# Optimization experiments

Hardware: AMD Instinct MI355X
Metric: run time of the kernel (lower is better)

Reference implementation:

```python
import jax, jax.numpy as jnp
from jax import lax
import numpy as np

B, T, D_IN, H, D_L1_IN = 128, 2048, 5, 128, 256


def _gru_layer(x, w_ih, w_hh, b_ih, b_hh, reverse):
    # x: [B,T,D]; w_ih: [3H,D]; w_hh: [3H,H]. PyTorch gate order: r, z, n.
    gx = jnp.einsum('btd,gd->btg', x, w_ih) + b_ih  # [B,T,3H] input projections, batched
    if reverse:
        gx = gx[:, ::-1]
    gx_t = jnp.swapaxes(gx, 0, 1)  # [T,B,3H]
    h0 = jnp.zeros((x.shape[0], H), x.dtype)

    def step(h, gxt):
        gh = h @ w_hh.T + b_hh  # [B,3H]
        r = jax.nn.sigmoid(gxt[:, :H] + gh[:, :H])
        z = jax.nn.sigmoid(gxt[:, H:2 * H] + gh[:, H:2 * H])
        n = jnp.tanh(gxt[:, 2 * H:] + r * gh[:, 2 * H:])
        h_new = (1.0 - z) * n + z * h
        return h_new, h_new

    _, ys = lax.scan(step, h0, gx_t)  # ys: [T,B,H]
    ys = jnp.swapaxes(ys, 0, 1)  # [B,T,H]
    if reverse:
        ys = ys[:, ::-1]
    return ys


def setup_inputs() -> dict:
    key = jax.random.key(0)
    ks = jax.random.split(key, 16)
    s0 = 1.0 / np.sqrt(H)

    def w(k, shape):
        return jax.random.uniform(k, shape, jnp.float32, -s0, s0)

    inp = {'seq': jax.random.normal(ks[0], (B, T, D_IN), jnp.float32)}
    # layer 0 forward / backward (input dim 5)
    inp['w_ih_l0f'] = w(ks[1], (3 * H, D_IN)); inp['w_hh_l0f'] = w(ks[2], (3 * H, H))
    inp['b_ih_l0f'] = w(ks[3], (3 * H,));      inp['b_hh_l0f'] = w(ks[4], (3 * H,))
    inp['w_ih_l0b'] = w(ks[5], (3 * H, D_IN)); inp['w_hh_l0b'] = w(ks[6], (3 * H, H))
    inp['b_ih_l0b'] = w(ks[7], (3 * H,));      inp['b_hh_l0b'] = w(ks[8], (3 * H,))
    # layer 1 forward / backward (input dim 256 = 2*H)
    inp['w_ih_l1f'] = w(ks[9], (3 * H, D_L1_IN));  inp['w_hh_l1f'] = w(ks[10], (3 * H, H))
    inp['b_ih_l1f'] = w(ks[11], (3 * H,));         inp['b_hh_l1f'] = w(ks[12], (3 * H,))
    inp['w_ih_l1b'] = w(ks[13], (3 * H, D_L1_IN)); inp['w_hh_l1b'] = w(ks[14], (3 * H, H))
    inp['b_ih_l1b'] = w(ks[15], (3 * H,));         inp['b_hh_l1b'] = w(ks[15], (3 * H,)) * 0.9
    # linear head
    kf = jax.random.split(ks[0], 2)
    inp['fc_w'] = w(kf[0], (1, 2 * H))
    inp['fc_b'] = w(kf[1], (1,))
    return inp


def reference(seq, w_ih_l0f, w_hh_l0f, b_ih_l0f, b_hh_l0f,
              w_ih_l0b, w_hh_l0b, b_ih_l0b, b_hh_l0b,
              w_ih_l1f, w_hh_l1f, b_ih_l1f, b_hh_l1f,
              w_ih_l1b, w_hh_l1b, b_ih_l1b, b_hh_l1b,
              fc_w, fc_b):
    # layer 0: bidirectional, concat directions
    y0f = _gru_layer(seq, w_ih_l0f, w_hh_l0f, b_ih_l0f, b_hh_l0f, reverse=False)
    y0b = _gru_layer(seq, w_ih_l0b, w_hh_l0b, b_ih_l0b, b_hh_l0b, reverse=True)
    y0 = jnp.concatenate([y0f, y0b], axis=-1)  # [B,T,256]
    # layer 1
    y1f = _gru_layer(y0, w_ih_l1f, w_hh_l1f, b_ih_l1f, b_hh_l1f, reverse=False)
    y1b = _gru_layer(y0, w_ih_l1b, w_hh_l1b, b_ih_l1b, b_hh_l1b, reverse=True)
    y1 = jnp.concatenate([y1f, y1b], axis=-1)  # [B,T,256]
    # head on last timestep
    return y1[:, -1, :] @ fc_w.T + fc_b  # [B,1]
```

## Files before the change

### kernel.cpp

```cpp
#include <hip/hip_runtime.h>
#include <hip/hip_fp16.h>
#include <cstdint>

#define B_   128
#define T_   2048
#define DIN  5
#define H_   128
#define G3   384
#define D1   256
#define CH   256
#define NCH  (T_ / CH)

typedef _Float16 half8 __attribute__((ext_vector_type(8)));
typedef float f32x4 __attribute__((ext_vector_type(4)));

__device__ __forceinline__ float sigmoid_f(float x) {
    return __builtin_amdgcn_rcpf(1.0f + __expf(-x));
}
__device__ __forceinline__ float tanh_f(float x) {
    return 1.0f - 2.0f * __builtin_amdgcn_rcpf(__expf(2.0f * x) + 1.0f);
}
__device__ __forceinline__ unsigned long long pack4h(const float* h) {
    union { __half2 h2[2]; unsigned long long u; } pk;
    pk.h2[0] = __floats2half2_rn(h[0], h[1]);
    pk.h2[1] = __floats2half2_rn(h[2], h[3]);
    return pk.u;
}
__device__ __forceinline__ f32x4 h4_to_f(unsigned long long u) {
    union { unsigned long long u; __half2 h2[2]; } p; p.u = u;
    const float2 a = __half22float2(p.h2[0]);
    const float2 b = __half22float2(p.h2[1]);
    f32x4 r; r[0] = a.x; r[1] = a.y; r[2] = b.x; r[3] = b.y; return r;
}
__device__ __forceinline__ void fast_barrier() {
    asm volatile("s_waitcnt lgkmcnt(0)\n\ts_barrier" ::: "memory");
}

__global__ __launch_bounds__(256, 1) void scan0_mfma3(
    const float* __restrict__ seq,
    const float* __restrict__ wihf, const float* __restrict__ whhf,
    const float* __restrict__ bihf, const float* __restrict__ bhhf,
    const float* __restrict__ wihb, const float* __restrict__ whhb,
    const float* __restrict__ bihb, const float* __restrict__ bhhb,
    __half* __restrict__ y0)
{
    const int tid = threadIdx.x;
    const int w  = tid >> 6;
    const int l  = tid & 63;
    const int lo = l & 15;
    const int g  = l >> 4;
    const int dir = blockIdx.x >> 3;
    const int bg  = blockIdx.x & 7;

    const float* w_ih = dir ? wihb : wihf;
    const float* w_hh = dir ? whhb : whhf;
    const float* b_ih = dir ? bihb : bihf;
    const float* b_hh = dir ? bhhb : bhhf;

    __shared__ __align__(16) char smem[2 * 16 * 512];

    half8 a_r[2][5], a_z[2][5], a_n[2][5], a_x[2];
#pragma unroll
    for (int i = 0; i < 2; ++i) {
        const int grow = (2 * w + i) * 16 + lo;
#pragma unroll
        for (int c = 0; c < 5; ++c) {
            half8 vr, vz, vn;
#pragma unroll
            for (int j = 0; j < 8; ++j) {
                const int k = c * 32 + g * 8 + j;
                float fr, fz, fn;
                if (k < 128) {
                    fr = w_hh[grow * H_ + k];
                    fz = w_hh[(128 + grow) * H_ + k];
                    fn = w_hh[(256 + grow) * H_ + k];
                } else if (k < 133) {
                    fr = w_ih[grow * DIN + (k - 128)];
                    fz = w_ih[(128 + grow) * DIN + (k - 128)];
                    fn = 0.f;
                } else if (k == 133) {
                    fr = b_ih[grow] + b_hh[grow];
                    fz = b_ih[128 + grow] + b_hh[128 + grow];
                    fn = b_hh[256 + grow];
                } else { fr = 0.f; fz = 0.f; fn = 0.f; }
                vr[j] = (_Float16)fr; vz[j] = (_Float16)fz; vn[j] = (_Float16)fn;
            }
            a_r[i][c] = vr; a_z[i][c] = vz; a_n[i][c] = vn;
        }
        half8 vx;
#pragma unroll
        for (int j = 0; j < 8; ++j) {
            const int k = 128 + g * 8 + j;
            float f = 0.f;
            if (k < 133)       f = w_ih[(256 + grow) * DIN + (k - 128)];
            else if (k == 133) f = b_ih[256 + grow];
            vx[j] = (_Float16)f;
        }
        a_x[i] = vx;
    }

#pragma unroll
    for (int q = 0; q < 4; ++q) {
        f32x4 z = {0.f, 0.f, 0.f, 0.f};
        *reinterpret_cast<f32x4*>(smem + tid * 64 + q * 16) = z;
    }
    __syncthreads();
    if (tid < 32) {
        const int row = tid & 15, bu = tid >> 4;
        *(_Float16*)(smem + bu * 8192 + row * 512 + (266 ^ ((row & 7) << 4))) =
            (_Float16)1.0f;
    }
    const bool stager = tid < 80;
    const int sb = tid / 5, sd = tid % 5;
    const size_t seqbase = (size_t)(bg * 16 + sb) * T_ * DIN + sd;
    float x_t1 = 0.f;
    if (stager) {
        const int tt0 = dir ? (T_ - 1) : 0;
        const float x0 = seq[seqbase + (size_t)tt0 * DIN];
        *(_Float16*)(smem + sb * 512 + ((256 + 2 * sd) ^ ((sb & 7) << 4))) =
            (_Float16)x0;
        const int tt1 = dir ? (T_ - 2) : 1;
        x_t1 = seq[seqbase + (size_t)tt1 * DIN];
    }
    __syncthreads();

    float h_old[2][4];
#pragma unroll
    for (int i = 0; i < 2; ++i)
#pragma unroll
        for (int q = 0; q < 4; ++q) h_old[i][q] = 0.f;

    for (int t = 0; t < T_; ++t) {
        char* cur = smem + (t & 1) * 8192;
        char* nxt = smem + ((t + 1) & 1) * 8192;

        if (stager)
            *(_Float16*)(nxt + sb * 512 + ((256 + 2 * sd) ^ ((sb & 7) << 4))) =
                (_Float16)x_t1;

        half8 bf[5];
#pragma unroll
        for (int c = 0; c < 5; ++c)
            bf[c] = *reinterpret_cast<const half8*>(
                cur + lo * 512 + ((c * 64 + g * 16) ^ ((lo & 7) << 4)));

        float x_t2 = 0.f;
        if (stager) {
            const int t2 = (t + 2 < T_) ? t + 2 : T_ - 1;
            const int tt2 = dir ? (T_ - 1 - t2) : t2;
            x_t2 = seq[seqbase + (size_t)tt2 * DIN];
        }

        f32x4 accr[2], accz[2], accn[2], accx[2];
#pragma unroll
        for (int i = 0; i < 2; ++i) {
            f32x4 zr = {0.f, 0.f, 0.f, 0.f};
            accr[i] = zr; accz[i] = zr; accn[i] = zr;
#pragma unroll
            for (int c = 0; c < 5; ++c) {
                accr[i] = __builtin_amdgcn_mfma_f32_16x16x32_f16(a_r[i][c], bf[c], accr[i], 0, 0, 0);
                accz[i] = __builtin_amdgcn_mfma_f32_16x16x32_f16(a_z[i][c], bf[c], accz[i], 0, 0, 0);
                accn[i] = __builtin_amdgcn_mfma_f32_16x16x32_f16(a_n[i][c], bf[c], accn[i], 0, 0, 0);
            }
            accx[i] = __builtin_amdgcn_mfma_f32_16x16x32_f16(a_x[i], bf[4], zr, 0, 0, 0);
        }

        const int tt = dir ? (T_ - 1 - t) : t;
#pragma unroll
        for (int i = 0; i < 2; ++i) {
            float hn[4];
#pragma unroll
            for (int q = 0; q < 4; ++q) {
                const float r = sigmoid_f(accr[i][q]);
                const float z = sigmoid_f(accz[i][q]);
                const float n = tanh_f(accx[i][q] + r * accn[i][q]);
                hn[q] = n + z * (h_old[i][q] - n);
                h_old[i][q] = hn[q];
            }
            const int j0 = (2 * w + i) * 16 + g * 4;
            const unsigned long long pu = pack4h(hn);
            *reinterpret_cast<unsigned long long*>(
                &y0[((size_t)(bg * 16 + lo) * T_ + tt) * D1 + dir * H_ + j0]) = pu;
            *reinterpret_cast<unsigned long long*>(
                nxt + lo * 512 + ((2 * j0) ^ ((lo & 7) << 4))) = pu;
        }
        x_t1 = x_t2;
        fast_barrier();
    }
}

__global__ __launch_bounds__(256, 2) void gemm1_f16(
    const __half* __restrict__ A,
    const float* __restrict__ W,
    const float* __restrict__ bias,
    __half* __restrict__ C,
    int c0)
{
    __shared__ __align__(16) _Float16 As[128][32];
    __shared__ __align__(16) _Float16 Bs[64][32];
    const int tid = threadIdx.x;
    const int wave = tid >> 6, l = tid & 63;
    const int wm = wave >> 1, wn = wave & 1;
    const int lo = l & 15, g = l >> 4;
    const int m0 = blockIdx.x * 128, n0 = blockIdx.y * 64;

    f32x4 acc[4][2];
#pragma unroll
    for (int mt = 0; mt < 4; ++mt)
#pragma unroll
        for (int nt = 0; nt < 2; ++nt) {
            f32x4 z = {0.f, 0.f, 0.f, 0.f};
            acc[mt][nt] = z;
        }

    for (int kc = 0; kc < 256; kc += 32) {
#pragma unroll
        for (int r2 = 0; r2 < 2; ++r2) {
            const int idx = tid + r2 * 256;
            const int row = idx >> 2, seg = idx & 3;
            const int m = m0 + row, bb = m >> 8, tlq = m & (CH - 1);
            const __half* src = A + ((size_t)bb * T_ + c0 + tlq) * D1 + kc + seg * 8;
            *reinterpret_cast<uint4*>(&As[row][seg * 8]) =
                *reinterpret_cast<const uint4*>(src);
        }
        {
            const int row = tid >> 2, seg = tid & 3;
            const float* srcw = W + (size_t)(n0 + row) * D1 + kc + seg * 8;
            const float4 u0 = *reinterpret_cast<const float4*>(srcw);
            const float4 u1 = *reinterpret_cast<const float4*>(srcw + 4);
            half8 hv;
            hv[0] = (_Float16)u0.x; hv[1] = (_Float16)u0.y;
            hv[2] = (_Float16)u0.z; hv[3] = (_Float16)u0.w;
            hv[4] = (_Float16)u1.x; hv[5] = (_Float16)u1.y;
            hv[6] = (_Float16)u1.z; hv[7] = (_Float16)u1.w;
            *reinterpret_cast<half8*>(&Bs[row][seg * 8]) = hv;
        }
        __syncthreads();
        half8 af[4], bfr[2];
#pragma unroll
        for (int mt = 0; mt < 4; ++mt)
            af[mt] = *reinterpret_cast<half8*>(&As[wm * 64 + mt * 16 + lo][g * 8]);
#pragma unroll
        for (int nt = 0; nt < 2; ++nt)
            bfr[nt] = *reinterpret_cast<half8*>(&Bs[wn * 32 + nt * 16 + lo][g * 8]);
#pragma unroll
        for (int mt = 0; mt < 4; ++mt)
#pragma unroll
            for (int nt = 0; nt < 2; ++nt)
                acc[mt][nt] = __builtin_amdgcn_mfma_f32_16x16x32_f16(
                    af[mt], bfr[nt], acc[mt][nt], 0, 0, 0);
        __syncthreads();
    }
#pragma unroll
    for (int nt = 0; nt < 2; ++nt) {
        const int n = n0 + wn * 32 + nt * 16 + lo;
        const float bv = bias[n];
#pragma unroll
        for (int mt = 0; mt < 4; ++mt) {
            const int mrow = m0 + wm * 64 + mt * 16 + g * 4;
#pragma unroll
            for (int q = 0; q < 4; ++q)
                C[(size_t)(mrow + q) * G3 + n] = __float2half(acc[mt][nt][q] + bv);
        }
    }
}

__global__ __launch_bounds__(256, 1) void scan1_mfma3(
    const __half* __restrict__ gxc,
    const float* __restrict__ whh, const float* __restrict__ bhh,
    float* __restrict__ h1, int c)
{
    const int tid = threadIdx.x;
    const int w = tid >> 6, l = tid & 63;
    const int lo = l & 15, g = l >> 4;
    const int grp = blockIdx.x;

    __shared__ __align__(16) char smem[2 * 16 * 256];

    half8 a_r[2][4], a_z[2][4], a_n[2][4];
    float br[2][4], bz[2][4], bn[2][4];
#pragma unroll
    for (int i = 0; i < 2; ++i) {
        const int grow = (2 * w + i) * 16 + lo;
#pragma unroll
        for (int cc = 0; cc < 4; ++cc) {
            half8 vr, vz, vn;
#pragma unroll
            for (int j = 0; j < 8; ++j) {
                const int k = cc * 32 + g * 8 + j;
                vr[j] = (_Float16)whh[grow * H_ + k];
                vz[j] = (_Float16)whh[(128 + grow) * H_ + k];
                vn[j] = (_Float16)whh[(256 + grow) * H_ + k];
            }
            a_r[i][cc] = vr; a_z[i][cc] = vz; a_n[i][cc] = vn;
        }
#pragma unroll
        for (int q = 0; q < 4; ++q) {
            const int gq = (2 * w + i) * 16 + g * 4 + q;
            br[i][q] = bhh[gq];
            bz[i][q] = bhh[128 + gq];
            bn[i][q] = bhh[256 + gq];
        }
    }

#pragma unroll
    for (int q = 0; q < 2; ++q) {
        f32x4 z = {0.f, 0.f, 0.f, 0.f};
        *reinterpret_cast<f32x4*>(smem + tid * 32 + q * 16) = z;
    }
    __syncthreads();

    float h_old[2][4];
    if (c == 0) {
#pragma unroll
        for (int i = 0; i < 2; ++i)
#pragma unroll
            for (int q = 0; q < 4; ++q) h_old[i][q] = 0.f;
    } else {
#pragma unroll
        for (int i = 0; i < 2; ++i) {
            const int j0 = (2 * w + i) * 16 + g * 4;
            const f32x4 hv = *reinterpret_cast<const f32x4*>(
                &h1[(grp * 16 + lo) * H_ + j0]);
            float hn[4];
#pragma unroll
            for (int q = 0; q < 4; ++q) { h_old[i][q] = hv[q]; hn[q] = hv[q]; }
            *reinterpret_cast<unsigned long long*>(
                smem + lo * 256 + ((2 * j0) ^ ((lo & 7) << 4))) = pack4h(hn);
        }
    }
    __syncthreads();

    const __half* gxl = gxc + (size_t)(grp * 16 + lo) * CH * G3;
    unsigned long long gxc_cur[6], gxc_nxt[6];
#pragma unroll
    for (int i = 0; i < 2; ++i) {
        const int gr0 = (2 * w + i) * 16 + g * 4;
        gxc_cur[i]     = *reinterpret_cast<const unsigned long long*>(gxl + gr0);
        gxc_cur[2 + i] = *reinterpret_cast<const unsigned long long*>(gxl + 128 + gr0);
        gxc_cur[4 + i] = *reinterpret_cast<const unsigned long long*>(gxl + 256 + gr0);
    }

    for (int t = 0; t < CH; ++t) {
        char* curb = smem + (t & 1) * 4096;
        char* nxtb = smem + ((t + 1) & 1) * 4096;

        half8 bf[4];
#pragma unroll
        for (int cc = 0; cc < 4; ++cc)
            bf[cc] = *reinterpret_cast<const half8*>(
                curb + lo * 256 + ((cc * 64 + g * 16) ^ ((lo & 7) << 4)));

        const int tn = (t + 1 < CH) ? t + 1 : t;
        const __half* p = gxl + (size_t)tn * G3;
#pragma unroll
        for (int i = 0; i < 2; ++i) {
            const int gr0 = (2 * w + i) * 16 + g * 4;
            gxc_nxt[i]     = *reinterpret_cast<const unsigned long long*>(p + gr0);
            gxc_nxt[2 + i] = *reinterpret_cast<const unsigned long long*>(p + 128 + gr0);
            gxc_nxt[4 + i] = *reinterpret_cast<const unsigned long long*>(p + 256 + gr0);
        }

        f32x4 accr[2], accz[2], accn[2];
#pragma unroll
        for (int i = 0; i < 2; ++i) {
            f32x4 zr = {0.f, 0.f, 0.f, 0.f};
            accr[i] = zr; accz[i] = zr; accn[i] = zr;
#pragma unroll
            for (int cc = 0; cc < 4; ++cc) {
                accr[i] = __builtin_amdgcn_mfma_f32_16x16x32_f16(a_r[i][cc], bf[cc], accr[i], 0, 0, 0);
                accz[i] = __builtin_amdgcn_mfma_f32_16x16x32_f16(a_z[i][cc], bf[cc], accz[i], 0, 0, 0);
                accn[i] = __builtin_amdgcn_mfma_f32_16x16x32_f16(a_n[i][cc], bf[cc], accn[i], 0, 0, 0);
            }
        }

#pragma unroll
        for (int i = 0; i < 2; ++i) {
            const f32x4 gr = h4_to_f(gxc_cur[i]);
            const f32x4 gz = h4_to_f(gxc_cur[2 + i]);
            const f32x4 gn = h4_to_f(gxc_cur[4 + i]);
            float hn[4];
#pragma unroll
            for (int q = 0; q < 4; ++q) {
                const float r = sigmoid_f(accr[i][q] + br[i][q] + gr[q]);
                const float z = sigmoid_f(accz[i][q] + bz[i][q] + gz[q]);
                const float n = tanh_f(gn[q] + r * (accn[i][q] + bn[i][q]));
                hn[q] = n + z * (h_old[i][q] - n);
                h_old[i][q] = hn[q];
            }
            const int j0 = (2 * w + i) * 16 + g * 4;
            *reinterpret_cast<unsigned long long*>(
                nxtb + lo * 256 + ((2 * j0) ^ ((lo & 7) << 4))) = pack4h(hn);
        }
#pragma unroll
        for (int i = 0; i < 6; ++i) gxc_cur[i] = gxc_nxt[i];
        fast_barrier();
    }

#pragma unroll
    for (int i = 0; i < 2; ++i) {
        const int j0 = (2 * w + i) * 16 + g * 4;
        f32x4 hv;
#pragma unroll
        for (int q = 0; q < 4; ++q) hv[q] = h_old[i][q];
        *reinterpret_cast<f32x4*>(&h1[(grp * 16 + lo) * H_ + j0]) = hv;
    }
}

__global__ __launch_bounds__(384, 1) void back1_fc(
    const __half* __restrict__ y0, const float* __restrict__ h1,
    const float* __restrict__ w_ih_1b, const float* __restrict__ b_ih_1b,
    const float* __restrict__ b_hh_1b,
    const float* __restrict__ fc_w, const float* __restrict__ fc_b,
    float* __restrict__ out)
{
    const int g = threadIdx.x;
    const int b = blockIdx.x;
    __shared__ float ylast[D1];
    __shared__ float pre_rz[2 * H_];
    __shared__ float gxn[H_], ghn[H_];
    __shared__ float hb[H_];
    __shared__ float red[H_];

    if (g < D1) ylast[g] = __half2float(y0[((size_t)b * T_ + (T_ - 1)) * D1 + g]);
    __syncthreads();

    float accb = b_ih_1b[g];
    const float* wrow = w_ih_1b + (size_t)g * D1;
#pragma unroll 8
    for (int k = 0; k < D1; k += 4) {
        const float4 v = *reinterpret_cast<const float4*>(&ylast[k]);
        const float4 wv = *reinterpret_cast<const float4*>(&wrow[k]);
        accb += v.x * wv.x + v.y * wv.y + v.z * wv.z + v.w * wv.w;
    }
    const float bh2 = b_hh_1b[g];
    if (g < 2 * H_) pre_rz[g] = accb + bh2;
    else            { gxn[g - 2 * H_] = accb; ghn[g - 2 * H_] = bh2; }
    __syncthreads();
    if (g < H_) {
        const float r = sigmoid_f(pre_rz[g]);
        const float z = sigmoid_f(pre_rz[g + H_]);
        const float n = tanh_f(gxn[g] + r * ghn[g]);
        hb[g] = (1.0f - z) * n;
    }
    __syncthreads();
    if (g < H_) red[g] = h1[b * H_ + g] * fc_w[g] + hb[g] * fc_w[H_ + g];
    __syncthreads();
    if (g == 0) {
        float s = fc_b[0];
#pragma unroll 8
        for (int k = 0; k < H_; ++k) s += red[k];
        out[b] = s;
    }
}

extern "C" void kernel_launch(void* const* d_in, const int* in_sizes, int n_in,
                              void* d_out, int out_size, void* d_ws, size_t ws_size,
                              hipStream_t stream)
{
    const float* seq      = (const float*)d_in[0];
    const float* w_ih_l0f = (const float*)d_in[1];
    const float* w_hh_l0f = (const float*)d_in[2];
    const float* b_ih_l0f = (const float*)d_in[3];
    const float* b_hh_l0f = (const float*)d_in[4];
    const float* w_ih_l0b = (const float*)d_in[5];
    const float* w_hh_l0b = (const float*)d_in[6];
    const float* b_ih_l0b = (const float*)d_in[7];
    const float* b_hh_l0b = (const float*)d_in[8];
    const float* w_ih_l1f = (const float*)d_in[9];
    const float* w_hh_l1f = (const float*)d_in[10];
    const float* b_ih_l1f = (const float*)d_in[11];
    const float* b_hh_l1f = (const float*)d_in[12];
    const float* w_ih_l1b = (const float*)d_in[13];
    const float* b_ih_l1b = (const float*)d_in[15];
    const float* b_hh_l1b = (const float*)d_in[16];
    const float* fc_w     = (const float*)d_in[17];
    const float* fc_b     = (const float*)d_in[18];
    float* out = (float*)d_out;

    __half* y0h = (__half*)d_ws;
    __half* gxc = (__half*)((char*)d_ws +
                  (size_t)B_ * T_ * D1 * sizeof(__half));
    float*  h1  = (float*)(gxc + (size_t)B_ * CH * G3);

    hipLaunchKernelGGL(scan0_mfma3, dim3(16), dim3(256), 0, stream,
        seq, w_ih_l0f, w_hh_l0f, b_ih_l0f, b_hh_l0f,
             w_ih_l0b, w_hh_l0b, b_ih_l0b, b_hh_l0b, y0h);

    for (int ci = 0; ci < NCH; ++ci) {
        hipLaunchKernelGGL(gemm1_f16, dim3(B_ * CH / 128, 6), dim3(256), 0, stream,
            y0h, w_ih_l1f, b_ih_l1f, gxc, ci * CH);
        hipLaunchKernelGGL(scan1_mfma3, dim3(8), dim3(256), 0, stream,
            gxc, w_hh_l1f, b_hh_l1f, h1, ci);
    }

    hipLaunchKernelGGL(back1_fc, dim3(B_), dim3(384), 0, stream,
        y0h, h1, w_ih_l1b, b_ih_l1b, b_hh_l1b, fc_w, fc_b, out);
}
```

Before: 3.666 ms.

## Split recurrent scans across eight waves with one gate tile per wave

Both recurrent scan kernels now launch 512 threads (8 waves), and each wave owns a single 16-row gate tile rather than two. The aim is to shorten the serial per-timestep chain of MFMAs and gate math each wave runs, spreading it across more SIMDs. The cost is a barrier across more waves on every timestep, and the 8 extra waves read the same shared h buffer. The scan0 stager logic and the zeroing of shared memory are adjusted to match the new thread count.

After: 3.890 ms. +6.1%, slower.

```diff
diff --git a/kernel.cpp b/kernel.cpp
--- a/kernel.cpp
+++ b/kernel.cpp
@@ -36,7 +36,7 @@
     asm volatile("s_waitcnt lgkmcnt(0)\n\ts_barrier" ::: "memory");
 }
 
-__global__ __launch_bounds__(256, 1) void scan0_mfma3(
+__global__ __launch_bounds__(512, 2) void scan0_mfma4(
     const float* __restrict__ seq,
     const float* __restrict__ wihf, const float* __restrict__ whhf,
     const float* __restrict__ bihf, const float* __restrict__ bhhf,
@@ -59,10 +59,9 @@
 
     __shared__ __align__(16) char smem[2 * 16 * 512];
 
-    half8 a_r[2][5], a_z[2][5], a_n[2][5], a_x[2];
-#pragma unroll
-    for (int i = 0; i < 2; ++i) {
-        const int grow = (2 * w + i) * 16 + lo;
+    half8 a_r[5], a_z[5], a_n[5], a_x;
+    {
+        const int grow = w * 16 + lo;
 #pragma unroll
         for (int c = 0; c < 5; ++c) {
             half8 vr, vz, vn;
@@ -85,7 +84,7 @@
                 } else { fr = 0.f; fz = 0.f; fn = 0.f; }
                 vr[j] = (_Float16)fr; vz[j] = (_Float16)fz; vn[j] = (_Float16)fn;
             }
-            a_r[i][c] = vr; a_z[i][c] = vz; a_n[i][c] = vn;
+            a_r[c] = vr; a_z[c] = vz; a_n[c] = vn;
         }
         half8 vx;
 #pragma unroll
@@ -96,13 +95,13 @@
             else if (k == 133) f = b_ih[256 + grow];
             vx[j] = (_Float16)f;
         }
-        a_x[i] = vx;
-    }
-
-#pragma unroll
-    for (int q = 0; q < 4; ++q) {
+        a_x = vx;
+    }
+
+#pragma unroll
+    for (int q = 0; q < 2; ++q) {
         f32x4 z = {0.f, 0.f, 0.f, 0.f};
-        *reinterpret_cast<f32x4*>(smem + tid * 64 + q * 16) = z;
+        *reinterpret_cast<f32x4*>(smem + tid * 32 + q * 16) = z;
     }
     __syncthreads();
     if (tid < 32) {
@@ -124,11 +123,9 @@
     }
     __syncthreads();
 
-    float h_old[2][4];
-#pragma unroll
-    for (int i = 0; i < 2; ++i)
-#pragma unroll
-        for (int q = 0; q < 4; ++q) h_old[i][q] = 0.f;
+    float h_old[4];
+#pragma unroll
+    for (int q = 0; q < 4; ++q) h_old[q] = 0.f;
 
     for (int t = 0; t < T_; ++t) {
         char* cur = smem + (t & 1) * 8192;
@@ -151,33 +148,28 @@
             x_t2 = seq[seqbase + (size_t)tt2 * DIN];
         }
 
-        f32x4 accr[2], accz[2], accn[2], accx[2];
-#pragma unroll
-        for (int i = 0; i < 2; ++i) {
-            f32x4 zr = {0.f, 0.f, 0.f, 0.f};
-            accr[i] = zr; accz[i] = zr; accn[i] = zr;
-#pragma unroll
-            for (int c = 0; c < 5; ++c) {
-                accr[i] = __builtin_amdgcn_mfma_f32_16x16x32_f16(a_r[i][c], bf[c], accr[i], 0, 0, 0);
-                accz[i] = __builtin_amdgcn_mfma_f32_16x16x32_f16(a_z[i][c], bf[c], accz[i], 0, 0, 0);
-                accn[i] = __builtin_amdgcn_mfma_f32_16x16x32_f16(a_n[i][c], bf[c], accn[i], 0, 0, 0);
+        f32x4 zr = {0.f, 0.f, 0.f, 0.f};
+        f32x4 accr = zr, accz = zr, accn = zr, accx;
+#pragma unroll
+        for (int c = 0; c < 5; ++c) {
+            accr = __builtin_amdgcn_mfma_f32_16x16x32_f16(a_r[c], bf[c], accr, 0, 0, 0);
+            accz = __builtin_amdgcn_mfma_f32_16x16x32_f16(a_z[c], bf[c], accz, 0, 0, 0);
+            accn = __builtin_amdgcn_mfma_f32_16x16x32_f16(a_n[c], bf[c], accn, 0, 0, 0);
+        }
+        accx = __builtin_amdgcn_mfma_f32_16x16x32_f16(a_x, bf[4], zr, 0, 0, 0);
+
+        const int tt = dir ? (T_ - 1 - t) : t;
+        {
+            float hn[4];
+#pragma unroll
+            for (int q = 0; q < 4; ++q) {
+                const float r = sigmoid_f(accr[q]);
+                const float z = sigmoid_f(accz[q]);
+                const float n = tanh_f(accx[q] + r * accn[q]);
+                hn[q] = n + z * (h_old[q] - n);
+                h_old[q] = hn[q];
             }
-            accx[i] = __builtin_amdgcn_mfma_f32_16x16x32_f16(a_x[i], bf[4], zr, 0, 0, 0);
-        }
-
-        const int tt = dir ? (T_ - 1 - t) : t;
-#pragma unroll
-        for (int i = 0; i < 2; ++i) {
-            float hn[4];
-#pragma unroll
-            for (int q = 0; q < 4; ++q) {
-                const float r = sigmoid_f(accr[i][q]);
-                const float z = sigmoid_f(accz[i][q]);
-                const float n = tanh_f(accx[i][q] + r * accn[i][q]);
-                hn[q] = n + z * (h_old[i][q] - n);
-                h_old[i][q] = hn[q];
-            }
-            const int j0 = (2 * w + i) * 16 + g * 4;
+            const int j0 = w * 16 + g * 4;
             const unsigned long long pu = pack4h(hn);
             *reinterpret_cast<unsigned long long*>(
                 &y0[((size_t)(bg * 16 + lo) * T_ + tt) * D1 + dir * H_ + j0]) = pu;
@@ -265,7 +257,7 @@
     }
 }
 
-__global__ __launch_bounds__(256, 1) void scan1_mfma3(
+__global__ __launch_bounds__(512, 2) void scan1_mfma4(
     const __half* __restrict__ gxc,
     const float* __restrict__ whh, const float* __restrict__ bhh,
     float* __restrict__ h1, int c)
@@ -277,11 +269,10 @@
 
     __shared__ __align__(16) char smem[2 * 16 * 256];
 
-    half8 a_r[2][4], a_z[2][4], a_n[2][4];
-    float br[2][4], bz[2][4], bn[2][4];
-#pragma unroll
-    for (int i = 0; i < 2; ++i) {
-        const int grow = (2 * w + i) * 16 + lo;
+    half8 a_r[4], a_z[4], a_n[4];
+    float br[4], bz[4], bn[4];
+    {
+        const int grow = w * 16 + lo;
 #pragma unroll
         for (int cc = 0; cc < 4; ++cc) {
             half8 vr, vz, vn;
@@ -292,53 +283,46 @@
                 vz[j] = (_Float16)whh[(128 + grow) * H_ + k];
                 vn[j] = (_Float16)whh[(256 + grow) * H_ + k];
             }
-            a_r[i][cc] = vr; a_z[i][cc] = vz; a_n[i][cc] = vn;
+            a_r[cc] = vr; a_z[cc] = vz; a_n[cc] = vn;
         }
 #pragma unroll
         for (int q = 0; q < 4; ++q) {
-            const int gq = (2 * w + i) * 16 + g * 4 + q;
-            br[i][q] = bhh[gq];
-            bz[i][q] = bhh[128 + gq];
-            bn[i][q] = bhh[256 + gq];
-        }
-    }
-
-#pragma unroll
-    for (int q = 0; q < 2; ++q) {
+            const int gq = w * 16 + g * 4 + q;
+            br[q] = bhh[gq];
+            bz[q] = bhh[128 + gq];
+            bn[q] = bhh[256 + gq];
+        }
+    }
+
+    {
         f32x4 z = {0.f, 0.f, 0.f, 0.f};
-        *reinterpret_cast<f32x4*>(smem + tid * 32 + q * 16) = z;
-    }
-    __syncthreads();
-
-    float h_old[2][4];
+        *reinterpret_cast<f32x4*>(smem + tid * 16) = z;
+    }
+    __syncthreads();
+
+    float h_old[4];
     if (c == 0) {
 #pragma unroll
-        for (int i = 0; i < 2; ++i)
-#pragma unroll
-            for (int q = 0; q < 4; ++q) h_old[i][q] = 0.f;
+        for (int q = 0; q < 4; ++q) h_old[q] = 0.f;
     } else {
-#pragma unroll
-        for (int i = 0; i < 2; ++i) {
-            const int j0 = (2 * w + i) * 16 + g * 4;
-            const f32x4 hv = *reinterpret_cast<const f32x4*>(
-                &h1[(grp * 16 + lo) * H_ + j0]);
-            float hn[4];
-#pragma unroll
-            for (int q = 0; q < 4; ++q) { h_old[i][q] = hv[q]; hn[q] = hv[q]; }
-            *reinterpret_cast<unsigned long long*>(
-                smem + lo * 256 + ((2 * j0) ^ ((lo & 7) << 4))) = pack4h(hn);
-        }
+        const int j0 = w * 16 + g * 4;
+        const f32x4 hv = *reinterpret_cast<const f32x4*>(
+            &h1[(grp * 16 + lo) * H_ + j0]);
+        float hn[4];
+#pragma unroll
+        for (int q = 0; q < 4; ++q) { h_old[q] = hv[q]; hn[q] = hv[q]; }
+        *reinterpret_cast<unsigned long long*>(
+            smem + lo * 256 + ((2 * j0) ^ ((lo & 7) << 4))) = pack4h(hn);
     }
     __syncthreads();
 
     const __half* gxl = gxc + (size_t)(grp * 16 + lo) * CH * G3;
-    unsigned long long gxc_cur[6], gxc_nxt[6];
-#pragma unroll
-    for (int i = 0; i < 2; ++i) {
-        const int gr0 = (2 * w + i) * 16 + g * 4;
-        gxc_cur[i]     = *reinterpret_cast<const unsigned long long*>(gxl + gr0);
-        gxc_cur[2 + i] = *reinterpret_cast<const unsigned long long*>(gxl + 128 + gr0);
-        gxc_cur[4 + i] = *reinterpret_cast<const unsigned long long*>(gxl + 256 + gr0);
+    unsigned long long gxc_cur[3], gxc_nxt[3];
+    {
+        const int gr0 = w * 16 + g * 4;
+        gxc_cur[0] = *reinterpret_cast<const unsigned long long*>(gxl + gr0);
+        gxc_cur[1] = *reinterpret_cast<const unsigned long long*>(gxl + 128 + gr0);
+        gxc_cur[2] = *reinterpret_cast<const unsigned long long*>(gxl + 256 + gr0);
     }
 
     for (int t = 0; t < CH; ++t) {
@@ -353,56 +337,49 @@
 
         const int tn = (t + 1 < CH) ? t + 1 : t;
         const __half* p = gxl + (size_t)tn * G3;
-#pragma unroll
-        for (int i = 0; i < 2; ++i) {
-            const int gr0 = (2 * w + i) * 16 + g * 4;
-            gxc_nxt[i]     = *reinterpret_cast<const unsigned long long*>(p + gr0);
-            gxc_nxt[2 + i] = *reinterpret_cast<const unsigned long long*>(p + 128 + gr0);
-            gxc_nxt[4 + i] = *reinterpret_cast<const unsigned long long*>(p + 256 + gr0);
-        }
-
-        f32x4 accr[2], accz[2], accn[2];
-#pragma unroll
-        for (int i = 0; i < 2; ++i) {
-            f32x4 zr = {0.f, 0.f, 0.f, 0.f};
-            accr[i] = zr; accz[i] = zr; accn[i] = zr;
-#pragma unroll
-            for (int cc = 0; cc < 4; ++cc) {
-                accr[i] = __builtin_amdgcn_mfma_f32_16x16x32_f16(a_r[i][cc], bf[cc], accr[i], 0, 0, 0);
-                accz[i] = __builtin_amdgcn_mfma_f32_16x16x32_f16(a_z[i][cc], bf[cc], accz[i], 0, 0, 0);
-                accn[i] = __builtin_amdgcn_mfma_f32_16x16x32_f16(a_n[i][cc], bf[cc], accn[i], 0, 0, 0);
+        {
+            const int gr0 = w * 16 + g * 4;
+            gxc_nxt[0] = *reinterpret_cast<const unsigned long long*>(p + gr0);
+            gxc_nxt[1] = *reinterpret_cast<const unsigned long long*>(p + 128 + gr0);
+            gxc_nxt[2] = *reinterpret_cast<const unsigned long long*>(p + 256 + gr0);
+        }
+
+        f32x4 zr = {0.f, 0.f, 0.f, 0.f};
+        f32x4 accr = zr, accz = zr, accn = zr;
+#pragma unroll
+        for (int cc = 0; cc < 4; ++cc) {
+            accr = __builtin_amdgcn_mfma_f32_16x16x32_f16(a_r[cc], bf[cc], accr, 0, 0, 0);
+            accz = __builtin_amdgcn_mfma_f32_16x16x32_f16(a_z[cc], bf[cc], accz, 0, 0, 0);
+            accn = __builtin_amdgcn_mfma_f32_16x16x32_f16(a_n[cc], bf[cc], accn, 0, 0, 0);
+        }
+
+        {
+            const f32x4 gr = h4_to_f(gxc_cur[0]);
+            const f32x4 gz = h4_to_f(gxc_cur[1]);
+            const f32x4 gn = h4_to_f(gxc_cur[2]);
+            float hn[4];
+#pragma unroll
+            for (int q = 0; q < 4; ++q) {
+                const float r = sigmoid_f(accr[q] + br[q] + gr[q]);
+                const float z = sigmoid_f(accz[q] + bz[q] + gz[q]);
+                const float n = tanh_f(gn[q] + r * (accn[q] + bn[q]));
+                hn[q] = n + z * (h_old[q] - n);
+                h_old[q] = hn[q];
             }
-        }
-
-#pragma unroll
-        for (int i = 0; i < 2; ++i) {
-            const f32x4 gr = h4_to_f(gxc_cur[i]);
-            const f32x4 gz = h4_to_f(gxc_cur[2 + i]);
-            const f32x4 gn = h4_to_f(gxc_cur[4 + i]);
-            float hn[4];
-#pragma unroll
-            for (int q = 0; q < 4; ++q) {
-                const float r = sigmoid_f(accr[i][q] + br[i][q] + gr[q]);
-                const float z = sigmoid_f(accz[i][q] + bz[i][q] + gz[q]);
-                const float n = tanh_f(gn[q] + r * (accn[i][q] + bn[i][q]));
-                hn[q] = n + z * (h_old[i][q] - n);
-                h_old[i][q] = hn[q];
-            }
-            const int j0 = (2 * w + i) * 16 + g * 4;
+            const int j0 = w * 16 + g * 4;
             *reinterpret_cast<unsigned long long*>(
                 nxtb + lo * 256 + ((2 * j0) ^ ((lo & 7) << 4))) = pack4h(hn);
         }
 #pragma unroll
-        for (int i = 0; i < 6; ++i) gxc_cur[i] = gxc_nxt[i];
+        for (int i = 0; i < 3; ++i) gxc_cur[i] = gxc_nxt[i];
         fast_barrier();
     }
 
-#pragma unroll
-    for (int i = 0; i < 2; ++i) {
-        const int j0 = (2 * w + i) * 16 + g * 4;
+    {
+        const int j0 = w * 16 + g * 4;
         f32x4 hv;
 #pragma unroll
-        for (int q = 0; q < 4; ++q) hv[q] = h_old[i][q];
+        for (int q = 0; q < 4; ++q) hv[q] = h_old[q];
         *reinterpret_cast<f32x4*>(&h1[(grp * 16 + lo) * H_ + j0]) = hv;
     }
 }
@@ -483,14 +460,14 @@
                   (size_t)B_ * T_ * D1 * sizeof(__half));
     float*  h1  = (float*)(gxc + (size_t)B_ * CH * G3);
 
-    hipLaunchKernelGGL(scan0_mfma3, dim3(16), dim3(256), 0, stream,
+    hipLaunchKernelGGL(scan0_mfma4, dim3(16), dim3(512), 0, stream,
         seq, w_ih_l0f, w_hh_l0f, b_ih_l0f, b_hh_l0f,
              w_ih_l0b, w_hh_l0b, b_ih_l0b, b_hh_l0b, y0h);
 
     for (int ci = 0; ci < NCH; ++ci) {
         hipLaunchKernelGGL(gemm1_f16, dim3(B_ * CH / 128, 6), dim3(256), 0, stream,
             y0h, w_ih_l1f, b_ih_l1f, gxc, ci * CH);
-        hipLaunchKernelGGL(scan1_mfma3, dim3(8), dim3(256), 0, stream,
+        hipLaunchKernelGGL(scan1_mfma4, dim3(8), dim3(512), 0, stream,
             gxc, w_hh_l1f, b_hh_l1f, h1, ci);
     }
 
```

## Widen layer-0 scan to 8 waves, split MFMA chains, run layer-1 unchunked

Applied to the files above, without the earlier changes.

The layer-0 scan now runs 512 threads per block, so each wave owns one 16-row gate tile instead of two. This halves the serial MFMA and activation work per wave on every timestep. In both scans the MFMA accumulation chains are split into independent partial accumulators that are summed afterwards, which shortens dependency latency. When the workspace is large enough, the layer-1 projection GEMM and forward scan each run once over the full sequence instead of in 8 chunks, removing launch overhead and per-chunk restarts at the cost of a larger workspace buffer.

Result: slower. 3.994 ms (+9.0%).

```diff
diff --git a/kernel.cpp b/kernel.cpp
--- a/kernel.cpp
+++ b/kernel.cpp
@@ -36,7 +36,7 @@
     asm volatile("s_waitcnt lgkmcnt(0)\n\ts_barrier" ::: "memory");
 }
 
-__global__ __launch_bounds__(256, 1) void scan0_mfma3(
+__global__ __launch_bounds__(512, 2) void scan0_mfma5(
     const float* __restrict__ seq,
     const float* __restrict__ wihf, const float* __restrict__ whhf,
     const float* __restrict__ bihf, const float* __restrict__ bhhf,
@@ -59,10 +59,9 @@
 
     __shared__ __align__(16) char smem[2 * 16 * 512];
 
-    half8 a_r[2][5], a_z[2][5], a_n[2][5], a_x[2];
-#pragma unroll
-    for (int i = 0; i < 2; ++i) {
-        const int grow = (2 * w + i) * 16 + lo;
+    half8 a_r[5], a_z[5], a_n[5], a_x;
+    {
+        const int grow = w * 16 + lo;
 #pragma unroll
         for (int c = 0; c < 5; ++c) {
             half8 vr, vz, vn;
@@ -85,7 +84,7 @@
                 } else { fr = 0.f; fz = 0.f; fn = 0.f; }
                 vr[j] = (_Float16)fr; vz[j] = (_Float16)fz; vn[j] = (_Float16)fn;
             }
-            a_r[i][c] = vr; a_z[i][c] = vz; a_n[i][c] = vn;
+            a_r[c] = vr; a_z[c] = vz; a_n[c] = vn;
         }
         half8 vx;
 #pragma unroll
@@ -96,13 +95,13 @@
             else if (k == 133) f = b_ih[256 + grow];
             vx[j] = (_Float16)f;
         }
-        a_x[i] = vx;
-    }
-
-#pragma unroll
-    for (int q = 0; q < 4; ++q) {
+        a_x = vx;
+    }
+
+#pragma unroll
+    for (int q = 0; q < 2; ++q) {
         f32x4 z = {0.f, 0.f, 0.f, 0.f};
-        *reinterpret_cast<f32x4*>(smem + tid * 64 + q * 16) = z;
+        *reinterpret_cast<f32x4*>(smem + tid * 32 + q * 16) = z;
     }
     __syncthreads();
     if (tid < 32) {
@@ -124,11 +123,9 @@
     }
     __syncthreads();
 
-    float h_old[2][4];
-#pragma unroll
-    for (int i = 0; i < 2; ++i)
-#pragma unroll
-        for (int q = 0; q < 4; ++q) h_old[i][q] = 0.f;
+    float h_old[4];
+#pragma unroll
+    for (int q = 0; q < 4; ++q) h_old[q] = 0.f;
 
     for (int t = 0; t < T_; ++t) {
         char* cur = smem + (t & 1) * 8192;
@@ -151,33 +148,43 @@
             x_t2 = seq[seqbase + (size_t)tt2 * DIN];
         }
 
-        f32x4 accr[2], accz[2], accn[2], accx[2];
-#pragma unroll
-        for (int i = 0; i < 2; ++i) {
-            f32x4 zr = {0.f, 0.f, 0.f, 0.f};
-            accr[i] = zr; accz[i] = zr; accn[i] = zr;
-#pragma unroll
-            for (int c = 0; c < 5; ++c) {
-                accr[i] = __builtin_amdgcn_mfma_f32_16x16x32_f16(a_r[i][c], bf[c], accr[i], 0, 0, 0);
-                accz[i] = __builtin_amdgcn_mfma_f32_16x16x32_f16(a_z[i][c], bf[c], accz[i], 0, 0, 0);
-                accn[i] = __builtin_amdgcn_mfma_f32_16x16x32_f16(a_n[i][c], bf[c], accn[i], 0, 0, 0);
+        f32x4 zr = {0.f, 0.f, 0.f, 0.f};
+        f32x4 ra = zr, rb = zr, rc = zr;
+        f32x4 za = zr, zb = zr, zc = zr;
+        f32x4 na = zr, nb = zr, nc = zr;
+        f32x4 accx;
+        ra = __builtin_amdgcn_mfma_f32_16x16x32_f16(a_r[0], bf[0], ra, 0, 0, 0);
+        za = __builtin_amdgcn_mfma_f32_16x16x32_f16(a_z[0], bf[0], za, 0, 0, 0);
+        na = __builtin_amdgcn_mfma_f32_16x16x32_f16(a_n[0], bf[0], na, 0, 0, 0);
+        rb = __builtin_amdgcn_mfma_f32_16x16x32_f16(a_r[2], bf[2], rb, 0, 0, 0);
+        zb = __builtin_amdgcn_mfma_f32_16x16x32_f16(a_z[2], bf[2], zb, 0, 0, 0);
+        nb = __builtin_amdgcn_mfma_f32_16x16x32_f16(a_n[2], bf[2], nb, 0, 0, 0);
+        ra = __builtin_amdgcn_mfma_f32_16x16x32_f16(a_r[1], bf[1], ra, 0, 0, 0);
+        za = __builtin_amdgcn_mfma_f32_16x16x32_f16(a_z[1], bf[1], za, 0, 0, 0);
+        na = __builtin_amdgcn_mfma_f32_16x16x32_f16(a_n[1], bf[1], na, 0, 0, 0);
+        rb = __builtin_amdgcn_mfma_f32_16x16x32_f16(a_r[3], bf[3], rb, 0, 0, 0);
+        zb = __builtin_amdgcn_mfma_f32_16x16x32_f16(a_z[3], bf[3], zb, 0, 0, 0);
+        nb = __builtin_amdgcn_mfma_f32_16x16x32_f16(a_n[3], bf[3], nb, 0, 0, 0);
+        rc = __builtin_amdgcn_mfma_f32_16x16x32_f16(a_r[4], bf[4], rc, 0, 0, 0);
+        zc = __builtin_amdgcn_mfma_f32_16x16x32_f16(a_z[4], bf[4], zc, 0, 0, 0);
+        nc = __builtin_amdgcn_mfma_f32_16x16x32_f16(a_n[4], bf[4], nc, 0, 0, 0);
+        accx = __builtin_amdgcn_mfma_f32_16x16x32_f16(a_x, bf[4], zr, 0, 0, 0);
+        const f32x4 accr = (ra + rb) + rc;
+        const f32x4 accz = (za + zb) + zc;
+        const f32x4 accn = (na + nb) + nc;
+
+        const int tt = dir ? (T_ - 1 - t) : t;
+        {
+            float hn[4];
+#pragma unroll
+            for (int q = 0; q < 4; ++q) {
+                const float r = sigmoid_f(accr[q]);
+                const float z = sigmoid_f(accz[q]);
+                const float n = tanh_f(accx[q] + r * accn[q]);
+                hn[q] = n + z * (h_old[q] - n);
+                h_old[q] = hn[q];
             }
-            accx[i] = __builtin_amdgcn_mfma_f32_16x16x32_f16(a_x[i], bf[4], zr, 0, 0, 0);
-        }
-
-        const int tt = dir ? (T_ - 1 - t) : t;
-#pragma unroll
-        for (int i = 0; i < 2; ++i) {
-            float hn[4];
-#pragma unroll
-            for (int q = 0; q < 4; ++q) {
-                const float r = sigmoid_f(accr[i][q]);
-                const float z = sigmoid_f(accz[i][q]);
-                const float n = tanh_f(accx[i][q] + r * accn[i][q]);
-                hn[q] = n + z * (h_old[i][q] - n);
-                h_old[i][q] = hn[q];
-            }
-            const int j0 = (2 * w + i) * 16 + g * 4;
+            const int j0 = w * 16 + g * 4;
             const unsigned long long pu = pack4h(hn);
             *reinterpret_cast<unsigned long long*>(
                 &y0[((size_t)(bg * 16 + lo) * T_ + tt) * D1 + dir * H_ + j0]) = pu;
@@ -194,7 +201,7 @@
     const float* __restrict__ W,
     const float* __restrict__ bias,
     __half* __restrict__ C,
-    int c0)
+    int c0, int log2L)
 {
     __shared__ __align__(16) _Float16 As[128][32];
     __shared__ __align__(16) _Float16 Bs[64][32];
@@ -203,6 +210,7 @@
     const int wm = wave >> 1, wn = wave & 1;
     const int lo = l & 15, g = l >> 4;
     const int m0 = blockIdx.x * 128, n0 = blockIdx.y * 64;
+    const int lmask = (1 << log2L) - 1;
 
     f32x4 acc[4][2];
 #pragma unroll
@@ -218,7 +226,7 @@
         for (int r2 = 0; r2 < 2; ++r2) {
             const int idx = tid + r2 * 256;
             const int row = idx >> 2, seg = idx & 3;
-            const int m = m0 + row, bb = m >> 8, tlq = m & (CH - 1);
+            const int m = m0 + row, bb = m >> log2L, tlq = m & lmask;
             const __half* src = A + ((size_t)bb * T_ + c0 + tlq) * D1 + kc + seg * 8;
             *reinterpret_cast<uint4*>(&As[row][seg * 8]) =
                 *reinterpret_cast<const uint4*>(src);
@@ -265,10 +273,10 @@
     }
 }
 
-__global__ __launch_bounds__(256, 1) void scan1_mfma3(
+__global__ __launch_bounds__(256, 1) void scan1_mfma5(
     const __half* __restrict__ gxc,
     const float* __restrict__ whh, const float* __restrict__ bhh,
-    float* __restrict__ h1, int c)
+    float* __restrict__ h1, int c, int L)
 {
     const int tid = threadIdx.x;
     const int w = tid >> 6, l = tid & 63;
@@ -331,7 +339,7 @@
     }
     __syncthreads();
 
-    const __half* gxl = gxc + (size_t)(grp * 16 + lo) * CH * G3;
+    const __half* gxl = gxc + (size_t)(grp * 16 + lo) * L * G3;
     unsigned long long gxc_cur[6], gxc_nxt[6];
 #pragma unroll
     for (int i = 0; i < 2; ++i) {
@@ -341,7 +349,7 @@
         gxc_cur[4 + i] = *reinterpret_cast<const unsigned long long*>(gxl + 256 + gr0);
     }
 
-    for (int t = 0; t < CH; ++t) {
+    for (int t = 0; t < L; ++t) {
         char* curb = smem + (t & 1) * 4096;
         char* nxtb = smem + ((t + 1) & 1) * 4096;
 
@@ -351,7 +359,7 @@
             bf[cc] = *reinterpret_cast<const half8*>(
                 curb + lo * 256 + ((cc * 64 + g * 16) ^ ((lo & 7) << 4)));
 
-        const int tn = (t + 1 < CH) ? t + 1 : t;
+        const int tn = (t + 1 < L) ? t + 1 : t;
         const __half* p = gxl + (size_t)tn * G3;
 #pragma unroll
         for (int i = 0; i < 2; ++i) {
@@ -365,13 +373,20 @@
 #pragma unroll
         for (int i = 0; i < 2; ++i) {
             f32x4 zr = {0.f, 0.f, 0.f, 0.f};
-            accr[i] = zr; accz[i] = zr; accn[i] = zr;
-#pragma unroll
-            for (int cc = 0; cc < 4; ++cc) {
-                accr[i] = __builtin_amdgcn_mfma_f32_16x16x32_f16(a_r[i][cc], bf[cc], accr[i], 0, 0, 0);
-                accz[i] = __builtin_amdgcn_mfma_f32_16x16x32_f16(a_z[i][cc], bf[cc], accz[i], 0, 0, 0);
-                accn[i] = __builtin_amdgcn_mfma_f32_16x16x32_f16(a_n[i][cc], bf[cc], accn[i], 0, 0, 0);
-            }
+            f32x4 rA = zr, rB = zr, zA = zr, zB = zr, nA = zr, nB = zr;
+            rA = __builtin_amdgcn_mfma_f32_16x16x32_f16(a_r[i][0], bf[0], rA, 0, 0, 0);
+            zA = __builtin_amdgcn_mfma_f32_16x16x32_f16(a_z[i][0], bf[0], zA, 0, 0, 0);
+            nA = __builtin_amdgcn_mfma_f32_16x16x32_f16(a_n[i][0], bf[0], nA, 0, 0, 0);
+            rB = __builtin_amdgcn_mfma_f32_16x16x32_f16(a_r[i][2], bf[2], rB, 0, 0, 0);
+            zB = __builtin_amdgcn_mfma_f32_16x16x32_f16(a_z[i][2], bf[2], zB, 0, 0, 0);
+            nB = __builtin_amdgcn_mfma_f32_16x16x32_f16(a_n[i][2], bf[2], nB, 0, 0, 0);
+            rA = __builtin_amdgcn_mfma_f32_16x16x32_f16(a_r[i][1], bf[1], rA, 0, 0, 0);
+            zA = __builtin_amdgcn_mfma_f32_16x16x32_f16(a_z[i][1], bf[1], zA, 0, 0, 0);
+            nA = __builtin_amdgcn_mfma_f32_16x16x32_f16(a_n[i][1], bf[1], nA, 0, 0, 0);
+            rB = __builtin_amdgcn_mfma_f32_16x16x32_f16(a_r[i][3], bf[3], rB, 0, 0, 0);
+            zB = __builtin_amdgcn_mfma_f32_16x16x32_f16(a_z[i][3], bf[3], zB, 0, 0, 0);
+            nB = __builtin_amdgcn_mfma_f32_16x16x32_f16(a_n[i][3], bf[3], nB, 0, 0, 0);
+            accr[i] = rA + rB; accz[i] = zA + zB; accn[i] = nA + nB;
         }
 
 #pragma unroll
@@ -478,22 +493,36 @@
     const float* fc_b     = (const float*)d_in[18];
     float* out = (float*)d_out;
 
+    const size_t y0_bytes   = (size_t)B_ * T_ * D1 * sizeof(__half);
+    const size_t gx_full_b  = (size_t)B_ * T_ * G3 * sizeof(__half);
+    const size_t gx_chunk_b = (size_t)B_ * CH * G3 * sizeof(__half);
+    const size_t h1_bytes   = (size_t)B_ * H_ * sizeof(float);
+
     __half* y0h = (__half*)d_ws;
-    __half* gxc = (__half*)((char*)d_ws +
-                  (size_t)B_ * T_ * D1 * sizeof(__half));
-    float*  h1  = (float*)(gxc + (size_t)B_ * CH * G3);
-
-    hipLaunchKernelGGL(scan0_mfma3, dim3(16), dim3(256), 0, stream,
+
+    hipLaunchKernelGGL(scan0_mfma5, dim3(16), dim3(512), 0, stream,
         seq, w_ih_l0f, w_hh_l0f, b_ih_l0f, b_hh_l0f,
              w_ih_l0b, w_hh_l0b, b_ih_l0b, b_hh_l0b, y0h);
 
-    for (int ci = 0; ci < NCH; ++ci) {
-        hipLaunchKernelGGL(gemm1_f16, dim3(B_ * CH / 128, 6), dim3(256), 0, stream,
-            y0h, w_ih_l1f, b_ih_l1f, gxc, ci * CH);
-        hipLaunchKernelGGL(scan1_mfma3, dim3(8), dim3(256), 0, stream,
-            gxc, w_hh_l1f, b_hh_l1f, h1, ci);
-    }
-
-    hipLaunchKernelGGL(back1_fc, dim3(B_), dim3(384), 0, stream,
-        y0h, h1, w_ih_l1b, b_ih_l1b, b_hh_l1b, fc_w, fc_b, out);
-}
+    if (ws_size >= y0_bytes + gx_full_b + h1_bytes) {
+        __half* gxc = (__half*)((char*)d_ws + y0_bytes);
+        float*  h1  = (float*)((char*)d_ws + y0_bytes + gx_full_b);
+        hipLaunchKernelGGL(gemm1_f16, dim3(B_ * T_ / 128, 6), dim3(256), 0, stream,
+            y0h, w_ih_l1f, b_ih_l1f, gxc, 0, 11 );
+        hipLaunchKernelGGL(scan1_mfma5, dim3(8), dim3(256), 0, stream,
+            gxc, w_hh_l1f, b_hh_l1f, h1, 0, T_);
+        hipLaunchKernelGGL(back1_fc, dim3(B_), dim3(384), 0, stream,
+            y0h, h1, w_ih_l1b, b_ih_l1b, b_hh_l1b, fc_w, fc_b, out);
+    } else {
+        __half* gxc = (__half*)((char*)d_ws + y0_bytes);
+        float*  h1  = (float*)((char*)d_ws + y0_bytes + gx_chunk_b);
+        for (int ci = 0; ci < NCH; ++ci) {
+            hipLaunchKernelGGL(gemm1_f16, dim3(B_ * CH / 128, 6), dim3(256), 0, stream,
+                y0h, w_ih_l1f, b_ih_l1f, gxc, ci * CH, 8 );
+            hipLaunchKernelGGL(scan1_mfma5, dim3(8), dim3(256), 0, stream,
+                gxc, w_hh_l1f, b_hh_l1f, h1, ci, CH);
+        }
+        hipLaunchKernelGGL(back1_fc, dim3(B_), dim3(384), 0, stream,
+            y0h, h1, w_ih_l1b, b_ih_l1b, b_hh_l1b, fc_w, fc_b, out);
+    }
+}
```
